# Performance work log

Measured on AMD Instinct MI355X. Metric: run time of the kernel, lower is better.

The kernel has to match this reference:

```python
import jax, jax.numpy as jnp
import numpy as np

ALPHA = 1.5      # entmax alpha (q parameter)
N_ITER = 50      # entmax-bisect iterations (entmax library default)
B, S, DM, H, HKV, HD = 1, 2048, 2048, 16, 4, 128
ROPE_THETA = 10000.0


def _entmax_p(x):
    """alpha-entmax along last axis via bisection on tau (matches entmax.EntmaxBisect)."""
    am1 = ALPHA - 1.0
    pw = 1.0 / am1
    X = x * am1
    d = x.shape[-1]
    max_val = jnp.max(X, axis=-1, keepdims=True)
    tau_lo = max_val - 1.0                      # _gp(1, alpha) = 1
    tau_hi = max_val - (1.0 / d) ** am1          # _gp(1/d, alpha)
    dm0 = tau_hi - tau_lo

    def body(i, carry):
        tau_lo, dm, tau_m = carry
        dm = dm * 0.5
        tau_m = tau_lo + dm
        p = jnp.maximum(X - tau_m, 0.0) ** pw
        f = jnp.sum(p, axis=-1, keepdims=True) - 1.0
        tau_lo = jnp.where(f >= 0, tau_m, tau_lo)
        return (tau_lo, dm, tau_m)

    tau_lo, dm, tau_m = jax.lax.fori_loop(0, N_ITER, body, (tau_lo, dm0, tau_lo))
    p = jnp.maximum(X - tau_m, 0.0) ** pw
    return p / jnp.sum(p, axis=-1, keepdims=True)  # ensure_sum_one


@jax.custom_vjp
def entmax_bisect(x):
    return _entmax_p(x)

def _emx_fwd(x):
    p = _entmax_p(x)
    return p, p

def _emx_bwd(p, g):
    # entmax library backward: gppr = p^(2-alpha) on support
    gppr = jnp.where(p > 0, p ** (2.0 - ALPHA), 0.0)
    dX = g * gppr
    q = jnp.sum(dX, axis=-1, keepdims=True) / jnp.sum(gppr, axis=-1, keepdims=True)
    return ((dX - q * gppr),)

entmax_bisect.defvjp(_emx_fwd, _emx_bwd)


def _rotate_half(x):
    x1, x2 = x[..., : HD // 2], x[..., HD // 2:]
    return jnp.concatenate([-x2, x1], axis=-1)


def setup_inputs() -> dict:
    key = jax.random.key(0)
    k1, k2, k3, k4, k5 = jax.random.split(key, 5)
    hidden_states = jax.random.normal(k1, (B, S, DM), dtype=jnp.float32)
    wq = jax.random.normal(k2, (H * HD, DM), dtype=jnp.float32) * 0.02
    wk = jax.random.normal(k3, (HKV * HD, DM), dtype=jnp.float32) * 0.02
    wv = jax.random.normal(k4, (HKV * HD, DM), dtype=jnp.float32) * 0.02
    wo = jax.random.normal(k5, (DM, H * HD), dtype=jnp.float32) * 0.02
    # real Llama RoPE position embeddings
    inv_freq = 1.0 / (ROPE_THETA ** (np.arange(0, HD, 2, dtype=np.float32) / HD))
    pos = np.arange(S, dtype=np.float32)
    freqs = pos[:, None] * inv_freq[None, :]          # [S, HD/2]
    emb = np.concatenate([freqs, freqs], axis=-1)     # [S, HD]
    cos = jnp.asarray(np.cos(emb))[None]              # [1, S, HD]
    sin = jnp.asarray(np.sin(emb))[None]
    return {"hidden_states": hidden_states, "cos": cos, "sin": sin,
            "wq": wq, "wk": wk, "wv": wv, "wo": wo}


def reference(hidden_states, cos, sin, wq, wk, wv, wo):
    b, s, _ = hidden_states.shape
    scaling = HD ** -0.5
    # QKV projections -> [B, H, S, HD]
    q = (hidden_states @ wq.T).reshape(b, s, H, HD).transpose(0, 2, 1, 3)
    k = (hidden_states @ wk.T).reshape(b, s, HKV, HD).transpose(0, 2, 1, 3)
    v = (hidden_states @ wv.T).reshape(b, s, HKV, HD).transpose(0, 2, 1, 3)
    # RoPE (cos/sin broadcast over head axis)
    c, sn = cos[:, None, :, :], sin[:, None, :, :]
    q = q * c + _rotate_half(q) * sn
    k = k * c + _rotate_half(k) * sn
    # GQA: repeat kv heads
    g = H // HKV
    k = jnp.repeat(k, g, axis=1)
    v = jnp.repeat(v, g, axis=1)
    scores = jnp.einsum('bhqd,bhkd->bhqk', q, k) * scaling
    causal = jnp.tril(jnp.ones((s, s), dtype=bool))
    scores = jnp.where(causal, scores, -jnp.inf)
    attn = entmax_bisect(scores)                      # [B, H, S, S]
    out = jnp.einsum('bhqk,bhkd->bhqd', attn, v)
    out = out.transpose(0, 2, 1, 3).reshape(b, s, H * HD)
    out = out @ wo.T
    return (out, attn)
```

## Files before the change

### kernel.cpp

```cpp
#include <hip/hip_runtime.h>

typedef __bf16 bf16;
typedef __bf16 bf16x4 __attribute__((ext_vector_type(4)));
typedef __bf16 bf16x8 __attribute__((ext_vector_type(8)));
typedef float f32x4 __attribute__((ext_vector_type(4)));

#define S 2048
#define DM 2048
#define HD 128
#define H 16
#define NQKV 3072
#define N_ITER_DEV 20

__device__ __forceinline__ void gl2lds16(const void* g, void* l) {
    __builtin_amdgcn_global_load_lds(
        (const __attribute__((address_space(1))) void*)g,
        (__attribute__((address_space(3))) void*)l, 16, 0, 0);
}

__device__ __forceinline__ void nt_store4(f32x4 v, float* p) {
    __builtin_nontemporal_store(v, (f32x4*)p);
}

__global__ void cvt_all(const float* __restrict__ hid, const float* __restrict__ wq,
                        const float* __restrict__ wk, const float* __restrict__ wv,
                        const float* __restrict__ wo, bf16* __restrict__ bh,
                        bf16* __restrict__ bqkv, bf16* __restrict__ bwo) {
    int i = blockIdx.x * blockDim.x + threadIdx.x;
    const float* src;
    bf16* dst;
    int off;
    if (i < 1048576) { src = hid; dst = bh; off = i; }
    else if (i < 2097152) { src = wq; dst = bqkv; off = i - 1048576; }
    else if (i < 2359296) { src = wk; dst = bqkv + 2048 * 2048; off = i - 2097152; }
    else if (i < 2621440) { src = wv; dst = bqkv + 2048 * 2048 + 512 * 2048; off = i - 2359296; }
    else { src = wo; dst = bwo; off = i - 2621440; }
    float4 f = ((const float4*)src)[off];
    bf16x4 o;
    o[0] = (bf16)f.x; o[1] = (bf16)f.y; o[2] = (bf16)f.z; o[3] = (bf16)f.w;
    ((bf16x4*)dst)[off] = o;
}

__global__ __launch_bounds__(256) void gemm128_bt(const bf16* __restrict__ A,
                                                  const bf16* __restrict__ B,
                                                  float* __restrict__ C, int Ndim, int K) {
    __shared__ bf16 As[128 * 32];
    __shared__ bf16 Bs[128 * 32];
    int m0 = blockIdx.x * 128, n0 = blockIdx.y * 128;
    int t = threadIdx.x;
    int l = t & 63, w = t >> 6;
    int lane16 = l & 15, quad = l >> 4;

    int c0 = (w * 2) * 64 + l;
    int c1 = c0 + 64;
    const bf16* Abase = A + (size_t)m0 * K;
    const bf16* Bbase = B + (size_t)n0 * K;

    int wm = (w & 1) * 64, wn = (w >> 1) * 64;
    f32x4 acc[4][4];
#pragma unroll
    for (int i = 0; i < 4; i++)
#pragma unroll
        for (int j = 0; j < 4; j++) acc[i][j] = (f32x4){0.f, 0.f, 0.f, 0.f};

    for (int k0 = 0; k0 < K; k0 += 32) {
        gl2lds16(Abase + (size_t)(c0 >> 2) * K + k0 + (c0 & 3) * 8, &As[(w * 2) * 512]);
        gl2lds16(Abase + (size_t)(c1 >> 2) * K + k0 + (c1 & 3) * 8, &As[(w * 2 + 1) * 512]);
        gl2lds16(Bbase + (size_t)(c0 >> 2) * K + k0 + (c0 & 3) * 8, &Bs[(w * 2) * 512]);
        gl2lds16(Bbase + (size_t)(c1 >> 2) * K + k0 + (c1 & 3) * 8, &Bs[(w * 2 + 1) * 512]);
        __syncthreads();
        bf16x8 af[4], bfr[4];
#pragma unroll
        for (int i = 0; i < 4; i++)
            af[i] = *(const bf16x8*)&As[(wm + i * 16 + lane16) * 32 + quad * 8];
#pragma unroll
        for (int j = 0; j < 4; j++)
            bfr[j] = *(const bf16x8*)&Bs[(wn + j * 16 + lane16) * 32 + quad * 8];
#pragma unroll
        for (int i = 0; i < 4; i++)
#pragma unroll
            for (int j = 0; j < 4; j++)
                acc[i][j] = __builtin_amdgcn_mfma_f32_16x16x32_bf16(af[i], bfr[j], acc[i][j], 0, 0, 0);
        __syncthreads();
    }
#pragma unroll
    for (int i = 0; i < 4; i++)
#pragma unroll
        for (int j = 0; j < 4; j++) {
            float* cp = C + (size_t)(m0 + wm + i * 16 + quad * 4) * Ndim + n0 + wn + j * 16 + lane16;
#pragma unroll
            for (int r = 0; r < 4; r++) cp[(size_t)r * Ndim] = acc[i][j][r];
        }
}

__global__ void rope_qk(const float* __restrict__ qkv, const float* __restrict__ cosb,
                        const float* __restrict__ sinb, bf16* __restrict__ qs,
                        bf16* __restrict__ kb) {
    int col = blockIdx.x * 256 + threadIdx.x;
    int s = blockIdx.y;
    const float* row = qkv + (size_t)s * NQKV;
    float v = row[col];
    if (col < DM) {
        int h = col >> 7, d = col & 127;
        float c = cosb[s * HD + d], sn = sinb[s * HD + d];
        float other = row[(h << 7) + ((d < 64) ? (d + 64) : (d - 64))];
        float rot = (d < 64) ? -other : other;
        float o = v * c + rot * sn;
        qs[((size_t)h * S + s) * HD + d] = (bf16)(o * 0.04419417382415922f);
    } else {
        int c2 = col - DM;
        int kv = c2 >> 7, d = c2 & 127;
        float c = cosb[s * HD + d], sn = sinb[s * HD + d];
        float other = row[DM + (kv << 7) + ((d < 64) ? (d + 64) : (d - 64))];
        float rot = (d < 64) ? -other : other;
        float o = v * c + rot * sn;
        kb[((size_t)kv * S + s) * HD + d] = (bf16)o;
    }
}

__global__ __launch_bounds__(256) void vtrans(const float* __restrict__ qkv, bf16* __restrict__ vT) {
    __shared__ bf16 tile[64][66];
    int s0 = blockIdx.x * 64, y0 = blockIdx.y * 64;
    int t = threadIdx.x;
    int ty = t & 63, tr = t >> 6;
#pragma unroll
    for (int i = 0; i < 16; i++) {
        int s = tr + i * 4;
        float v = qkv[(size_t)(s0 + s) * NQKV + 2560 + y0 + ty];
        tile[s][ty] = (bf16)v;
    }
    __syncthreads();
#pragma unroll
    for (int i = 0; i < 16; i++) {
        int y = tr + i * 4;
        vT[(size_t)(y0 + y) * S + s0 + ty] = tile[ty][y];
    }
}

template <int SEGS>
__device__ __forceinline__ void attn_body(const bf16* __restrict__ qs, const bf16* __restrict__ kb,
                                          const bf16* __restrict__ vT, float* __restrict__ attn,
                                          bf16* __restrict__ o, int r0, int h,
                                          float (&sc)[16][528], bf16 (&pb)[16][552]) {
    constexpr int NREG = SEGS * 8;
    int jlen = r0 + 16;
    int l = threadIdx.x & 63;
    int w = threadIdx.x >> 6;
    int lane16 = l & 15, quad = l >> 4;

    const bf16* qrow = qs + ((size_t)h * S + (r0 + lane16)) * HD + quad * 8;
    bf16x8 afrag[4];
#pragma unroll
    for (int kc = 0; kc < 4; kc++) afrag[kc] = *(const bf16x8*)(qrow + kc * 32);

    const bf16* kbase = kb + (size_t)(h >> 2) * S * HD;
    const bf16* vbase = vT + (size_t)(h >> 2) * HD * S;
    float xr[NREG];

#pragma unroll
    for (int sgi = 0; sgi < SEGS; sgi++) {
        int j0 = sgi * 512;
#pragma unroll
        for (int tt = 0; tt < 2; tt++) {
            int t = w + tt * 16;
            int jt = j0 + t * 16;
            if (jt < jlen) {
                f32x4 acc = {0.f, 0.f, 0.f, 0.f};
                const bf16* kp = kbase + (size_t)(jt + lane16) * HD + quad * 8;
#pragma unroll
                for (int kc = 0; kc < 4; kc++) {
                    bf16x8 b = *(const bf16x8*)(kp + kc * 32);
                    acc = __builtin_amdgcn_mfma_f32_16x16x32_bf16(afrag[kc], b, acc, 0, 0, 0);
                }
                int jj = jt + lane16;
#pragma unroll
                for (int r = 0; r < 4; r++) {
                    int rowi = quad * 4 + r;
                    float v = acc[r];
                    if (jj > r0 + rowi) v = -1e30f;
                    sc[rowi][t * 16 + lane16] = v;
                }
            }
        }
        __syncthreads();
#pragma unroll
        for (int part = 0; part < 2; part++) {
            float4 f = *(const float4*)&sc[w][part * 256 + l * 4];
            int jb = j0 + part * 256 + l * 4;
            xr[sgi * 8 + part * 4 + 0] = (jb + 0 < jlen) ? f.x : -1e30f;
            xr[sgi * 8 + part * 4 + 1] = (jb + 1 < jlen) ? f.y : -1e30f;
            xr[sgi * 8 + part * 4 + 2] = (jb + 2 < jlen) ? f.z : -1e30f;
            xr[sgi * 8 + part * 4 + 3] = (jb + 3 < jlen) ? f.w : -1e30f;
        }
        __syncthreads();
    }

    float m = -1e30f;
#pragma unroll
    for (int c = 0; c < NREG; c++) m = fmaxf(m, xr[c]);
#pragma unroll
    for (int off = 1; off < 64; off <<= 1) m = fmaxf(m, __shfl_xor(m, off));

    float tau_lo = m - 1.0f;
    float dmh = 0.97790291309f;
    float tau_m = tau_lo;
    for (int it = 0; it < N_ITER_DEV; it++) {
        dmh *= 0.5f;
        tau_m = tau_lo + dmh;
        float f = 0.f;
#pragma unroll
        for (int c = 0; c < NREG; c++) {
            float t = fmaxf(xr[c] - tau_m, 0.f);
            f = fmaf(t, t, f);
        }
#pragma unroll
        for (int off = 1; off < 64; off <<= 1) f += __shfl_xor(f, off);
        tau_lo = (f >= 1.0f) ? tau_m : tau_lo;
    }

    float ssum = 0.f;
#pragma unroll
    for (int c = 0; c < NREG; c++) {
        float t = fmaxf(xr[c] - tau_m, 0.f);
        ssum = fmaf(t, t, ssum);
    }
#pragma unroll
    for (int off = 1; off < 64; off <<= 1) ssum += __shfl_xor(ssum, off);
    float inv = 1.0f / ssum;

    int jt_o = (w & 7) * 16;
    int kh = (w >> 3) * 256;
    f32x4 acc_o = {0.f, 0.f, 0.f, 0.f};

#pragma unroll
    for (int sgi = 0; sgi < SEGS; sgi++) {
        int j0 = sgi * 512;
#pragma unroll
        for (int part = 0; part < 2; part++) {
            float t0 = fmaxf(xr[sgi * 8 + part * 4 + 0] - tau_m, 0.f);
            float t1 = fmaxf(xr[sgi * 8 + part * 4 + 1] - tau_m, 0.f);
            float t2 = fmaxf(xr[sgi * 8 + part * 4 + 2] - tau_m, 0.f);
            float t3 = fmaxf(xr[sgi * 8 + part * 4 + 3] - tau_m, 0.f);
            bf16x4 pbv;
            pbv[0] = (bf16)(t0 * t0 * inv); pbv[1] = (bf16)(t1 * t1 * inv);
            pbv[2] = (bf16)(t2 * t2 * inv); pbv[3] = (bf16)(t3 * t3 * inv);
            *(bf16x4*)&pb[w][part * 256 + l * 4] = pbv;
        }
        __syncthreads();
#pragma unroll
        for (int ks = 0; ks < 8; ks++) {
            int kk = kh + ks * 32;
            bf16x8 a = *(const bf16x8*)&pb[lane16][kk + quad * 8];
            bf16x8 b = *(const bf16x8*)(vbase + (size_t)(jt_o + lane16) * S + j0 + kk + quad * 8);
            acc_o = __builtin_amdgcn_mfma_f32_16x16x32_bf16(a, b, acc_o, 0, 0, 0);
        }
        __syncthreads();
    }

    if (w >= 8) {
#pragma unroll
        for (int r = 0; r < 4; r++) sc[w - 8][l * 4 + r] = acc_o[r];
    }
    __syncthreads();
    if (w < 8) {
        bf16* op = o + (size_t)(r0 + quad * 4) * DM + h * HD + jt_o + lane16;
#pragma unroll
        for (int r = 0; r < 4; r++) {
            float v = acc_o[r] + sc[w][l * 4 + r];
            op[(size_t)r * DM] = (bf16)v;
        }
    }

    float* arow = attn + ((size_t)h * S + (r0 + w)) * S;
#pragma unroll
    for (int sgi = 0; sgi < SEGS; sgi++) {
        int j0 = sgi * 512;
#pragma unroll
        for (int part = 0; part < 2; part++) {
            float t0 = fmaxf(xr[sgi * 8 + part * 4 + 0] - tau_m, 0.f);
            float t1 = fmaxf(xr[sgi * 8 + part * 4 + 1] - tau_m, 0.f);
            float t2 = fmaxf(xr[sgi * 8 + part * 4 + 2] - tau_m, 0.f);
            float t3 = fmaxf(xr[sgi * 8 + part * 4 + 3] - tau_m, 0.f);
            f32x4 pv;
            pv[0] = t0 * t0 * inv; pv[1] = t1 * t1 * inv;
            pv[2] = t2 * t2 * inv; pv[3] = t3 * t3 * inv;
            nt_store4(pv, &arow[j0 + part * 256 + l * 4]);
        }
    }
    f32x4 z4 = {0.f, 0.f, 0.f, 0.f};
    for (int j = SEGS * 512 + l * 4; j < S; j += 256) nt_store4(z4, &arow[j]);
}

__global__ __launch_bounds__(1024) void attn_av_all(const bf16* __restrict__ qs,
                                                    const bf16* __restrict__ kb,
                                                    const bf16* __restrict__ vT,
                                                    float* __restrict__ attn,
                                                    bf16* __restrict__ o) {
    __shared__ float sc[16][528];
    __shared__ bf16 pb[16][552];
    int qb = 127 - blockIdx.x;
    int h = blockIdx.y;
    int r0 = qb * 16;
    int nseg = (qb >> 5) + 1;
    switch (nseg) {
        case 1: attn_body<1>(qs, kb, vT, attn, o, r0, h, sc, pb); break;
        case 2: attn_body<2>(qs, kb, vT, attn, o, r0, h, sc, pb); break;
        case 3: attn_body<3>(qs, kb, vT, attn, o, r0, h, sc, pb); break;
        default: attn_body<4>(qs, kb, vT, attn, o, r0, h, sc, pb); break;
    }
}

extern "C" void kernel_launch(void* const* d_in, const int* in_sizes, int n_in,
                              void* d_out, int out_size, void* d_ws, size_t ws_size,
                              hipStream_t stream) {
    const float* hidden = (const float*)d_in[0];
    const float* cosb   = (const float*)d_in[1];
    const float* sinb   = (const float*)d_in[2];
    const float* wq     = (const float*)d_in[3];
    const float* wk     = (const float*)d_in[4];
    const float* wv     = (const float*)d_in[5];
    const float* wo     = (const float*)d_in[6];
    char* ws = (char*)d_ws;
    bf16*  bf_hidden = (bf16*)(ws);
    bf16*  bf_wqkv   = (bf16*)(ws + 8388608);
    bf16*  bf_wo     = (bf16*)(ws + 20971520);
    float* qkv_raw   = (float*)(ws + 29360128);
    bf16*  qsb       = (bf16*)(ws + 54525952);
    bf16*  kbb       = (bf16*)(ws + 62914560);
    bf16*  vTb       = (bf16*)(ws + 65011712);
    float* out  = (float*)d_out;
    float* attn = out + 4194304;

    cvt_all<<<dim3(14336), 256, 0, stream>>>(hidden, wq, wk, wv, wo, bf_hidden, bf_wqkv, bf_wo);

    gemm128_bt<<<dim3(16, 24), 256, 0, stream>>>(bf_hidden, bf_wqkv, qkv_raw, NQKV, DM);

    rope_qk<<<dim3(10, S), 256, 0, stream>>>(qkv_raw, cosb, sinb, qsb, kbb);
    vtrans<<<dim3(32, 8), 256, 0, stream>>>(qkv_raw, vTb);

    attn_av_all<<<dim3(128, H), 1024, 0, stream>>>(qsb, kbb, vTb, attn, bf_hidden);

    gemm128_bt<<<dim3(16, 16), 256, 0, stream>>>(bf_hidden, bf_wo, out, DM, DM);
}
```

Before: 661.9 us.

## Replace entmax bisection with Newton iterations and double-buffer score LDS

Replaces the 20-step bisection for the entmax threshold with 12 Newton steps on sum(relu(x-tau)^2)=1, using the derivative sum(relu(x-tau)). The per-step partial sums are split over four accumulators. The score and probability LDS buffers are merged into one double-buffered float array, which removes one barrier per segment in both the score phase and the AV phase. Causal masking is now skipped for tiles fully below the diagonal. Newton started from m-1 converges monotonically for this convex function, but 12 steps in fp32 may give a slightly different threshold than bisection.

Result: no change. 666.9 us (+0.7%).

```diff
diff --git a/kernel.cpp b/kernel.cpp
--- a/kernel.cpp
+++ b/kernel.cpp
@@ -10,7 +10,7 @@
 #define HD 128
 #define H 16
 #define NQKV 3072
-#define N_ITER_DEV 20
+#define NEWTON_ITERS 12
 
 __device__ __forceinline__ void gl2lds16(const void* g, void* l) {
     __builtin_amdgcn_global_load_lds(
@@ -141,7 +141,7 @@
 __device__ __forceinline__ void attn_body(const bf16* __restrict__ qs, const bf16* __restrict__ kb,
                                           const bf16* __restrict__ vT, float* __restrict__ attn,
                                           bf16* __restrict__ o, int r0, int h,
-                                          float (&sc)[16][528], bf16 (&pb)[16][552]) {
+                                          float (&buf)[2][16][532]) {
     constexpr int NREG = SEGS * 8;
     int jlen = r0 + 16;
     int l = threadIdx.x & 63;
@@ -160,6 +160,7 @@
 #pragma unroll
     for (int sgi = 0; sgi < SEGS; sgi++) {
         int j0 = sgi * 512;
+        float (*sb)[532] = buf[sgi & 1];
 #pragma unroll
         for (int tt = 0; tt < 2; tt++) {
             int t = w + tt * 16;
@@ -172,27 +173,42 @@
                     bf16x8 b = *(const bf16x8*)(kp + kc * 32);
                     acc = __builtin_amdgcn_mfma_f32_16x16x32_bf16(afrag[kc], b, acc, 0, 0, 0);
                 }
-                int jj = jt + lane16;
-#pragma unroll
-                for (int r = 0; r < 4; r++) {
-                    int rowi = quad * 4 + r;
-                    float v = acc[r];
-                    if (jj > r0 + rowi) v = -1e30f;
-                    sc[rowi][t * 16 + lane16] = v;
+                if (jt + 15 > r0) {
+                    int jj = jt + lane16;
+#pragma unroll
+                    for (int r = 0; r < 4; r++) {
+                        int rowi = quad * 4 + r;
+                        float v = acc[r];
+                        if (jj > r0 + rowi) v = -1e30f;
+                        sb[rowi][t * 16 + lane16] = v;
+                    }
+                } else {
+#pragma unroll
+                    for (int r = 0; r < 4; r++) sb[quad * 4 + r][t * 16 + lane16] = acc[r];
                 }
             }
         }
         __syncthreads();
-#pragma unroll
-        for (int part = 0; part < 2; part++) {
-            float4 f = *(const float4*)&sc[w][part * 256 + l * 4];
-            int jb = j0 + part * 256 + l * 4;
-            xr[sgi * 8 + part * 4 + 0] = (jb + 0 < jlen) ? f.x : -1e30f;
-            xr[sgi * 8 + part * 4 + 1] = (jb + 1 < jlen) ? f.y : -1e30f;
-            xr[sgi * 8 + part * 4 + 2] = (jb + 2 < jlen) ? f.z : -1e30f;
-            xr[sgi * 8 + part * 4 + 3] = (jb + 3 < jlen) ? f.w : -1e30f;
-        }
-        __syncthreads();
+        if (sgi == SEGS - 1) {
+#pragma unroll
+            for (int part = 0; part < 2; part++) {
+                float4 f = *(const float4*)&sb[w][part * 256 + l * 4];
+                int jb = j0 + part * 256 + l * 4;
+                xr[sgi * 8 + part * 4 + 0] = (jb + 0 < jlen) ? f.x : -1e30f;
+                xr[sgi * 8 + part * 4 + 1] = (jb + 1 < jlen) ? f.y : -1e30f;
+                xr[sgi * 8 + part * 4 + 2] = (jb + 2 < jlen) ? f.z : -1e30f;
+                xr[sgi * 8 + part * 4 + 3] = (jb + 3 < jlen) ? f.w : -1e30f;
+            }
+        } else {
+#pragma unroll
+            for (int part = 0; part < 2; part++) {
+                float4 f = *(const float4*)&sb[w][part * 256 + l * 4];
+                xr[sgi * 8 + part * 4 + 0] = f.x;
+                xr[sgi * 8 + part * 4 + 1] = f.y;
+                xr[sgi * 8 + part * 4 + 2] = f.z;
+                xr[sgi * 8 + part * 4 + 3] = f.w;
+            }
+        }
     }
 
     float m = -1e30f;
@@ -201,29 +217,37 @@
 #pragma unroll
     for (int off = 1; off < 64; off <<= 1) m = fmaxf(m, __shfl_xor(m, off));
 
-    float tau_lo = m - 1.0f;
-    float dmh = 0.97790291309f;
-    float tau_m = tau_lo;
-    for (int it = 0; it < N_ITER_DEV; it++) {
-        dmh *= 0.5f;
-        tau_m = tau_lo + dmh;
-        float f = 0.f;
-#pragma unroll
-        for (int c = 0; c < NREG; c++) {
-            float t = fmaxf(xr[c] - tau_m, 0.f);
-            f = fmaf(t, t, f);
-        }
-#pragma unroll
-        for (int off = 1; off < 64; off <<= 1) f += __shfl_xor(f, off);
-        tau_lo = (f >= 1.0f) ? tau_m : tau_lo;
-    }
-
-    float ssum = 0.f;
-#pragma unroll
-    for (int c = 0; c < NREG; c++) {
-        float t = fmaxf(xr[c] - tau_m, 0.f);
-        ssum = fmaf(t, t, ssum);
-    }
+    float tau = m - 1.0f;
+#pragma unroll 1
+    for (int it = 0; it < NEWTON_ITERS; it++) {
+        float f0 = 0.f, f1 = 0.f, f2 = 0.f, f3 = 0.f;
+        float g0 = 0.f, g1 = 0.f, g2 = 0.f, g3 = 0.f;
+#pragma unroll
+        for (int c = 0; c < NREG; c += 4) {
+            float t0 = fmaxf(xr[c + 0] - tau, 0.f); f0 = fmaf(t0, t0, f0); g0 += t0;
+            float t1 = fmaxf(xr[c + 1] - tau, 0.f); f1 = fmaf(t1, t1, f1); g1 += t1;
+            float t2 = fmaxf(xr[c + 2] - tau, 0.f); f2 = fmaf(t2, t2, f2); g2 += t2;
+            float t3 = fmaxf(xr[c + 3] - tau, 0.f); f3 = fmaf(t3, t3, f3); g3 += t3;
+        }
+        float f = (f0 + f1) + (f2 + f3);
+        float g = (g0 + g1) + (g2 + g3);
+#pragma unroll
+        for (int off = 1; off < 64; off <<= 1) {
+            f += __shfl_xor(f, off);
+            g += __shfl_xor(g, off);
+        }
+        tau += (f - 1.0f) / (2.0f * g + 1e-20f);
+    }
+
+    float s0 = 0.f, s1 = 0.f, s2 = 0.f, s3 = 0.f;
+#pragma unroll
+    for (int c = 0; c < NREG; c += 4) {
+        float t0 = fmaxf(xr[c + 0] - tau, 0.f); s0 = fmaf(t0, t0, s0);
+        float t1 = fmaxf(xr[c + 1] - tau, 0.f); s1 = fmaf(t1, t1, s1);
+        float t2 = fmaxf(xr[c + 2] - tau, 0.f); s2 = fmaf(t2, t2, s2);
+        float t3 = fmaxf(xr[c + 3] - tau, 0.f); s3 = fmaf(t3, t3, s3);
+    }
+    float ssum = (s0 + s1) + (s2 + s3);
 #pragma unroll
     for (int off = 1; off < 64; off <<= 1) ssum += __shfl_xor(ssum, off);
     float inv = 1.0f / ssum;
@@ -232,41 +256,43 @@
     int kh = (w >> 3) * 256;
     f32x4 acc_o = {0.f, 0.f, 0.f, 0.f};
 
+    __syncthreads();
 #pragma unroll
     for (int sgi = 0; sgi < SEGS; sgi++) {
         int j0 = sgi * 512;
+        bf16 (*pbf)[552] = (bf16(*)[552])(&buf[sgi & 1][0][0]);
 #pragma unroll
         for (int part = 0; part < 2; part++) {
-            float t0 = fmaxf(xr[sgi * 8 + part * 4 + 0] - tau_m, 0.f);
-            float t1 = fmaxf(xr[sgi * 8 + part * 4 + 1] - tau_m, 0.f);
-            float t2 = fmaxf(xr[sgi * 8 + part * 4 + 2] - tau_m, 0.f);
-            float t3 = fmaxf(xr[sgi * 8 + part * 4 + 3] - tau_m, 0.f);
+            float t0 = fmaxf(xr[sgi * 8 + part * 4 + 0] - tau, 0.f);
+            float t1 = fmaxf(xr[sgi * 8 + part * 4 + 1] - tau, 0.f);
+            float t2 = fmaxf(xr[sgi * 8 + part * 4 + 2] - tau, 0.f);
+            float t3 = fmaxf(xr[sgi * 8 + part * 4 + 3] - tau, 0.f);
             bf16x4 pbv;
             pbv[0] = (bf16)(t0 * t0 * inv); pbv[1] = (bf16)(t1 * t1 * inv);
             pbv[2] = (bf16)(t2 * t2 * inv); pbv[3] = (bf16)(t3 * t3 * inv);
-            *(bf16x4*)&pb[w][part * 256 + l * 4] = pbv;
+            *(bf16x4*)&pbf[w][part * 256 + l * 4] = pbv;
         }
         __syncthreads();
 #pragma unroll
         for (int ks = 0; ks < 8; ks++) {
             int kk = kh + ks * 32;
-            bf16x8 a = *(const bf16x8*)&pb[lane16][kk + quad * 8];
+            bf16x8 a = *(const bf16x8*)&pbf[lane16][kk + quad * 8];
             bf16x8 b = *(const bf16x8*)(vbase + (size_t)(jt_o + lane16) * S + j0 + kk + quad * 8);
             acc_o = __builtin_amdgcn_mfma_f32_16x16x32_bf16(a, b, acc_o, 0, 0, 0);
         }
-        __syncthreads();
-    }
-
+    }
+
+    __syncthreads();
     if (w >= 8) {
 #pragma unroll
-        for (int r = 0; r < 4; r++) sc[w - 8][l * 4 + r] = acc_o[r];
+        for (int r = 0; r < 4; r++) buf[0][w - 8][l * 4 + r] = acc_o[r];
     }
     __syncthreads();
     if (w < 8) {
         bf16* op = o + (size_t)(r0 + quad * 4) * DM + h * HD + jt_o + lane16;
 #pragma unroll
         for (int r = 0; r < 4; r++) {
-            float v = acc_o[r] + sc[w][l * 4 + r];
+            float v = acc_o[r] + buf[0][w][l * 4 + r];
             op[(size_t)r * DM] = (bf16)v;
         }
     }
@@ -277,10 +303,10 @@
         int j0 = sgi * 512;
 #pragma unroll
         for (int part = 0; part < 2; part++) {
-            float t0 = fmaxf(xr[sgi * 8 + part * 4 + 0] - tau_m, 0.f);
-            float t1 = fmaxf(xr[sgi * 8 + part * 4 + 1] - tau_m, 0.f);
-            float t2 = fmaxf(xr[sgi * 8 + part * 4 + 2] - tau_m, 0.f);
-            float t3 = fmaxf(xr[sgi * 8 + part * 4 + 3] - tau_m, 0.f);
+            float t0 = fmaxf(xr[sgi * 8 + part * 4 + 0] - tau, 0.f);
+            float t1 = fmaxf(xr[sgi * 8 + part * 4 + 1] - tau, 0.f);
+            float t2 = fmaxf(xr[sgi * 8 + part * 4 + 2] - tau, 0.f);
+            float t3 = fmaxf(xr[sgi * 8 + part * 4 + 3] - tau, 0.f);
             f32x4 pv;
             pv[0] = t0 * t0 * inv; pv[1] = t1 * t1 * inv;
             pv[2] = t2 * t2 * inv; pv[3] = t3 * t3 * inv;
@@ -296,17 +322,16 @@
                                                     const bf16* __restrict__ vT,
                                                     float* __restrict__ attn,
                                                     bf16* __restrict__ o) {
-    __shared__ float sc[16][528];
-    __shared__ bf16 pb[16][552];
+    __shared__ float buf[2][16][532];
     int qb = 127 - blockIdx.x;
     int h = blockIdx.y;
     int r0 = qb * 16;
     int nseg = (qb >> 5) + 1;
     switch (nseg) {
-        case 1: attn_body<1>(qs, kb, vT, attn, o, r0, h, sc, pb); break;
-        case 2: attn_body<2>(qs, kb, vT, attn, o, r0, h, sc, pb); break;
-        case 3: attn_body<3>(qs, kb, vT, attn, o, r0, h, sc, pb); break;
-        default: attn_body<4>(qs, kb, vT, attn, o, r0, h, sc, pb); break;
+        case 1: attn_body<1>(qs, kb, vT, attn, o, r0, h, buf); break;
+        case 2: attn_body<2>(qs, kb, vT, attn, o, r0, h, buf); break;
+        case 3: attn_body<3>(qs, kb, vT, attn, o, r0, h, buf); break;
+        default: attn_body<4>(qs, kb, vT, attn, o, r0, h, buf); break;
     }
 }
 
```
